# Performance work log

Measured on AMD Instinct MI355X. Metric: run time of the kernel, lower is better.

The kernel has to match this reference:

```python
import jax, jax.numpy as jnp
import numpy as np

N = 8192
D = 128
AVG_DEG = 32


def setup_inputs() -> dict:
    key = jax.random.key(0)
    ks = jax.random.split(key, 10)
    Z = jax.random.normal(ks[0], (N, D), dtype=jnp.float32)
    # random symmetric binary adjacency with avg degree ~ AVG_DEG
    p = AVG_DEG / N
    adj = (jax.random.uniform(ks[1], (N, N)) < p).astype(jnp.float32)
    adj = jnp.maximum(adj, adj.T)
    # symmetric normalized adjacency: D^{-1/2} A D^{-1/2}
    deg = adj.sum(axis=1)
    d_inv_sqrt = jnp.where(deg > 0, 1.0 / jnp.sqrt(deg), 0.0)
    A_norm = d_inv_sqrt[:, None] * adj * d_inv_sqrt[None, :]
    sc = 1.0 / np.sqrt(D)
    W_D = jax.random.uniform(ks[2], (D, D), minval=-sc, maxval=sc, dtype=jnp.float32)
    W_C = jax.random.uniform(ks[3], (D, D), minval=-sc, maxval=sc, dtype=jnp.float32)
    w_V = jax.random.uniform(ks[4], (D,), minval=-sc, maxval=sc, dtype=jnp.float32)
    W1 = jax.random.uniform(ks[5], (D, D), minval=-sc, maxval=sc, dtype=jnp.float32)
    b1 = jax.random.uniform(ks[6], (D,), minval=-sc, maxval=sc, dtype=jnp.float32)
    W2 = jax.random.uniform(ks[7], (D, D), minval=-sc, maxval=sc, dtype=jnp.float32)
    b2 = jax.random.uniform(ks[8], (D,), minval=-sc, maxval=sc, dtype=jnp.float32)
    omega_logit = jnp.float32(0.0)  # sigmoid -> 0.5
    delta_logit = jnp.float32(0.0)
    return {"Z": Z, "A_norm": A_norm, "W_D": W_D, "W_C": W_C, "w_V": w_V,
            "W1": W1, "b1": b1, "W2": W2, "b2": b2,
            "omega_logit": omega_logit, "delta_logit": delta_logit}


def reference(Z, A_norm, W_D, W_C, w_V, W1, b1, W2, b2, omega_logit, delta_logit):
    omega = jax.nn.sigmoid(omega_logit)
    delta = jax.nn.sigmoid(delta_logit)
    # Diffusion: ReLU(A_norm @ Z @ W_D^T)
    dif = jax.nn.relu(A_norm @ (Z @ W_D.T))  # [N, D]
    # Convection (standard attention). Since W_V is D->1,
    # W_V(z_i - z_j) == s_i - s_j with s = Z @ w_V -> avoid [N,N,D] tensor.
    s = Z @ w_V                                   # [N]
    V_bar = jax.nn.sigmoid(s[:, None] - s[None, :])  # [N, N]
    A = jax.nn.softmax(V_bar, axis=1)                # row-stochastic [N, N]
    con = A @ (Z @ W_C.T)                            # [N, D]
    # Reaction: nonlinear MLP
    rea = jnp.tanh(Z @ W1.T + b1) @ W2.T + b2        # [N, D]
    return omega * dif + (1.0 - omega) * con + delta * rea
```

## Files before the change

### kernel.cpp

```cpp
#include <hip/hip_runtime.h>
#include <hip/hip_bf16.h>
#include <stdint.h>

#define NN 8192
#define DD 128
#define MAXDEG 128

typedef float f32x4 __attribute__((ext_vector_type(4)));
typedef unsigned int u32x4 __attribute__((ext_vector_type(4)));
typedef __bf16 bf16x8 __attribute__((ext_vector_type(8)));
typedef __bf16 bf16x4 __attribute__((ext_vector_type(4)));

__device__ __forceinline__ f32x4 mfma16(bf16x8 a, bf16x8 b, f32x4 c) {
    return __builtin_amdgcn_mfma_f32_16x16x32_bf16(a, b, c, 0, 0, 0);
}

__device__ __forceinline__ bf16x8 pack8(f32x4 lo, f32x4 hi) {
    bf16x8 r;
    r[0] = (__bf16)lo[0]; r[1] = (__bf16)lo[1]; r[2] = (__bf16)lo[2]; r[3] = (__bf16)lo[3];
    r[4] = (__bf16)hi[0]; r[5] = (__bf16)hi[1]; r[6] = (__bf16)hi[2]; r[7] = (__bf16)hi[3];
    return r;
}

__device__ __forceinline__ float fast_sigmoid(float x) {
    return __builtin_amdgcn_rcpf(1.0f + __expf(-x));
}

__device__ __forceinline__ uint32_t f32_bf16bits_rne(float f) {
    union { float f; uint32_t u; } c; c.f = f;
    return (c.u + 0x7fffu + ((c.u >> 16) & 1u)) >> 16;
}

__device__ __forceinline__ float bf16bits_f32(uint32_t b) {
    union { uint32_t u; float f; } c; c.u = b << 16;
    return c.f;
}

__global__ __launch_bounds__(256) void k_prep_sE(
    const float* __restrict__ Z, const float* __restrict__ wV, float* __restrict__ E)
{
    const int wid  = threadIdx.x >> 6;
    const int lane = threadIdx.x & 63;
    const int row  = blockIdx.x * 4 + wid;
    float p = Z[row * DD + lane] * wV[lane] + Z[row * DD + 64 + lane] * wV[64 + lane];
    #pragma unroll
    for (int off = 32; off > 0; off >>= 1) p += __shfl_xor(p, off, 64);
    if (lane == 0) E[row] = __expf(p);
}

__global__ __launch_bounds__(256) void k_conv_w(
    const float* __restrict__ W_D, const float* __restrict__ W_C,
    const float* __restrict__ W1, const float* __restrict__ W2,
    __bf16* __restrict__ Wb)
{
    const int t = blockIdx.x * 256 + threadIdx.x;
    const int m = t >> 12, i = t & 4095;
    const float* src = (m == 0) ? W_D : (m == 1) ? W_C : (m == 2) ? W1 : W2;
    const f32x4 v = *(const f32x4*)(src + i * 4);
    bf16x4 b;
    b[0] = (__bf16)v[0]; b[1] = (__bf16)v[1]; b[2] = (__bf16)v[2]; b[3] = (__bf16)v[3];
    *(bf16x4*)(Wb + m * 16384 + i * 4) = b;
}

__global__ __launch_bounds__(256) void k_prep2(
    const float* __restrict__ Z, const __bf16* __restrict__ Wb,
    const float* __restrict__ b1, const float* __restrict__ b2,
    const float* __restrict__ delta_logit,
    __bf16* __restrict__ XR, __bf16* __restrict__ YB, __bf16* __restrict__ REA)
{
    __shared__ __bf16 Hs[32][136];
    const int tid = threadIdx.x;
    const int w = tid >> 6, l = tid & 63;
    const int lr = l & 15, lg = l >> 4;
    const int wr = w & 1, wn = w >> 1;
    const int r0 = blockIdx.x * 32;
    const int arow = r0 + 16 * wr + lr;
    const __bf16* WDb = Wb;
    const __bf16* WCb = Wb + 16384;
    const __bf16* W1b = Wb + 32768;
    const __bf16* W2b = Wb + 49152;

    const f32x4 zero4 = {0.f, 0.f, 0.f, 0.f};
    f32x4 aXD[4], aY[4], aH[4];
    #pragma unroll
    for (int i = 0; i < 4; ++i) { aXD[i] = zero4; aY[i] = zero4; aH[i] = zero4; }

    #pragma unroll
    for (int t = 0; t < 4; ++t) {
        const int k0 = 32 * t + 8 * lg;
        const bf16x8 af = pack8(*(const f32x4*)(Z + arow * DD + k0),
                                *(const f32x4*)(Z + arow * DD + k0 + 4));
        #pragma unroll
        for (int nf = 0; nf < 4; ++nf) {
            const int col = 64 * wn + 16 * nf + lr;
            aXD[nf] = mfma16(af, *(const bf16x8*)(WDb + col * DD + k0), aXD[nf]);
            aY[nf]  = mfma16(af, *(const bf16x8*)(WCb + col * DD + k0), aY[nf]);
            aH[nf]  = mfma16(af, *(const bf16x8*)(W1b + col * DD + k0), aH[nf]);
        }
    }

    const int orow = r0 + 16 * wr + 4 * lg;
    const int tile = orow >> 5;
    #pragma unroll
    for (int nf = 0; nf < 4; ++nf) {
        const int col = 64 * wn + 16 * nf + lr;
        bf16x4 yo;
        const float bb1 = b1[col];
        #pragma unroll
        for (int r = 0; r < 4; ++r) {
            XR[(orow + r) * DD + col] = (__bf16)aXD[nf][r];
            yo[r] = (__bf16)aY[nf][r];
            const float x = aH[nf][r] + bb1;
            const float e = __expf(2.0f * x);
            Hs[16 * wr + 4 * lg + r][col] = (__bf16)(1.0f - 2.0f * __builtin_amdgcn_rcpf(e + 1.0f));
        }
        *(bf16x4*)(YB + tile * 4096 + col * 32 + (orow & 31)) = yo;
    }
    __syncthreads();

    f32x4 aR[4];
    #pragma unroll
    for (int i = 0; i < 4; ++i) aR[i] = zero4;
    #pragma unroll
    for (int t = 0; t < 4; ++t) {
        const int k0 = 32 * t + 8 * lg;
        const bf16x8 hf = *(const bf16x8*)(&Hs[16 * wr + lr][k0]);
        #pragma unroll
        for (int nf = 0; nf < 4; ++nf) {
            const int col = 64 * wn + 16 * nf + lr;
            aR[nf] = mfma16(hf, *(const bf16x8*)(W2b + col * DD + k0), aR[nf]);
        }
    }
    const float delta = fast_sigmoid(delta_logit[0]);
    #pragma unroll
    for (int nf = 0; nf < 4; ++nf) {
        const int col = 64 * wn + 16 * nf + lr;
        const float bb2 = b2[col];
        #pragma unroll
        for (int r = 0; r < 4; ++r)
            REA[(orow + r) * DD + col] = (__bf16)(delta * (aR[nf][r] + bb2));
    }
}

__global__ __launch_bounds__(256) void k_scan(
    const float* __restrict__ A, uint32_t* __restrict__ cnt, uint32_t* __restrict__ ents)
{
    const int wid = threadIdx.x >> 6, lane = threadIdx.x & 63;
    const int row = blockIdx.x * 4 + wid;
    const float* rp = A + (size_t)row * NN + lane * 4;
    uint32_t* eb = ents + row * MAXDEG;
    uint32_t base = 0;
    #pragma unroll 4
    for (int i = 0; i < 32; ++i) {
        const f32x4 v = *(const f32x4*)(rp + i * 256);
        const int colb = i * 256 + lane * 4;
        #pragma unroll
        for (int k = 0; k < 4; ++k) {
            const bool nz = (v[k] != 0.0f);
            const unsigned long long m = __ballot(nz);
            if (nz) {
                const uint32_t pfx = __builtin_amdgcn_mbcnt_hi(
                    (uint32_t)(m >> 32), __builtin_amdgcn_mbcnt_lo((uint32_t)m, 0u));
                const uint32_t slot = base + pfx;
                if (slot < MAXDEG)
                    eb[slot] = ((uint32_t)(colb + k) << 16) | f32_bf16bits_rne(v[k]);
            }
            base += (uint32_t)__popcll(m);
        }
    }
    if (lane == 0) cnt[row] = base;
}

__global__ __launch_bounds__(512) __attribute__((amdgpu_waves_per_eu(2, 2))) void k_con(
    const float* __restrict__ E, const __bf16* __restrict__ YB,
    const __bf16* __restrict__ XR, const __bf16* __restrict__ REA,
    const uint32_t* __restrict__ cnt, const uint32_t* __restrict__ ents,
    const float* __restrict__ omega_logit, float* __restrict__ out)
{
    __shared__ float red[4][64][76];
    float* conS = &red[0][0][0];
    const int tid = threadIdx.x;
    const int w = tid >> 6, l = tid & 63;
    const int lr = l & 15, lg = l >> 4;
    const int r0 = blockIdx.x * 32;
    const int kstart = w * 1024;

    const float* ep = E + kstart + 8 * lg;
    const __bf16* yp = YB + (kstart >> 5) * 4096 + lr * 32 + 8 * lg;
    const float u0 = E[r0 + lr];
    const float u1 = E[r0 + 16 + lr];

    const f32x4 zero4 = {0.f, 0.f, 0.f, 0.f};
    f32x4 aC0[8], aC1[8], aden0 = zero4, aden1 = zero4;
    #pragma unroll
    for (int i = 0; i < 8; ++i) { aC0[i] = zero4; aC1[i] = zero4; }
    bf16x8 ones;
    #pragma unroll
    for (int i = 0; i < 8; ++i) ones[i] = (__bf16)1.0f;

    f32x4 eAa, eBa, eAb, eBb;
    bf16x8 bya[8], byb[8];
    intptr_t adv = 32;

#define LOADT(S) do {                                                         \
        eA##S = *(const f32x4*)(ep); eB##S = *(const f32x4*)(ep + 4);         \
        _Pragma("unroll")                                                     \
        for (int c = 0; c < 8; ++c) by##S[c] = *(const bf16x8*)(yp + c * 512);\
        ep += adv; yp += adv * 128;                                           \
    } while (0)

#define COMPT(S) do {                                                         \
        bf16x8 gf0, gf1;                                                      \
        _Pragma("unroll")                                                     \
        for (int j = 0; j < 4; ++j) {                                         \
            const float ea = eA##S[j], eb = eB##S[j];                         \
            gf0[j]     = (__bf16)__expf(u0 * __builtin_amdgcn_rcpf(u0 + ea)); \
            gf0[4 + j] = (__bf16)__expf(u0 * __builtin_amdgcn_rcpf(u0 + eb)); \
            gf1[j]     = (__bf16)__expf(u1 * __builtin_amdgcn_rcpf(u1 + ea)); \
            gf1[4 + j] = (__bf16)__expf(u1 * __builtin_amdgcn_rcpf(u1 + eb)); \
        }                                                                     \
        _Pragma("unroll")                                                     \
        for (int c = 0; c < 8; ++c) {                                         \
            aC0[c] = mfma16(gf0, by##S[c], aC0[c]);                           \
            aC1[c] = mfma16(gf1, by##S[c], aC1[c]);                           \
        }                                                                     \
        aden0 = mfma16(gf0, ones, aden0);                                     \
        aden1 = mfma16(gf1, ones, aden1);                                     \
    } while (0)

    LOADT(a);
    for (int it = 0; it < 16; ++it) {
        if (it == 15) adv = 0;
        LOADT(b); COMPT(a);
        LOADT(a); COMPT(b);
    }
#undef LOADT
#undef COMPT

#define STORE_ACC(dst) do {                                                   \
        _Pragma("unroll")                                                     \
        for (int c = 0; c < 8; ++c) {                                         \
            *(f32x4*)((dst) + c * 4)      = aC0[c];                           \
            *(f32x4*)((dst) + 36 + c * 4) = aC1[c];                           \
        }                                                                     \
        *(f32x4*)((dst) + 32)      = aden0;                                   \
        *(f32x4*)((dst) + 36 + 32) = aden1;                                   \
    } while (0)
#define ADD_ACC(src) do {                                                     \
        _Pragma("unroll")                                                     \
        for (int c = 0; c < 8; ++c) {                                         \
            aC0[c] += *(const f32x4*)((src) + c * 4);                         \
            aC1[c] += *(const f32x4*)((src) + 36 + c * 4);                    \
        }                                                                     \
        aden0 += *(const f32x4*)((src) + 32);                                 \
        aden1 += *(const f32x4*)((src) + 36 + 32);                            \
    } while (0)

    if (w >= 4) STORE_ACC(&red[w - 4][l][0]);
    __syncthreads();
    if (w < 4) ADD_ACC(&red[w][l][0]);
    __syncthreads();
    if (w == 2 || w == 3) STORE_ACC(&red[w - 2][l][0]);
    __syncthreads();
    if (w < 2) ADD_ACC(&red[w][l][0]);
    __syncthreads();
    if (w == 1) STORE_ACC(&red[0][l][0]);
    __syncthreads();
    if (w == 0) {
        ADD_ACC(&red[0][l][0]);
        __builtin_amdgcn_s_barrier();
        #pragma unroll
        for (int rf = 0; rf < 2; ++rf) {
            #pragma unroll
            for (int c = 0; c < 8; ++c) {
                const f32x4 v = rf ? aC1[c] : aC0[c];
                #pragma unroll
                for (int r = 0; r < 4; ++r)
                    conS[(16 * rf + 4 * lg + r) * 132 + 16 * c + lr] = v[r];
            }
            if (lr == 0) {
                const f32x4 d = rf ? aden1 : aden0;
                #pragma unroll
                for (int r = 0; r < 4; ++r)
                    conS[32 * 132 + 16 * rf + 4 * lg + r] = d[r];
            }
        }
    } else {
        __builtin_amdgcn_s_barrier();
    }
    __syncthreads();

    const int row = tid >> 4;
    const int g16 = tid & 15;
    const int col0 = 8 * g16;
    const int rg = r0 + row;
    float acc[8];
    #pragma unroll
    for (int i = 0; i < 8; ++i) acc[i] = 0.0f;

    const uint32_t n = min(cnt[rg], (uint32_t)MAXDEG);
    const uint32_t* ep2 = ents + rg * MAXDEG;
    uint32_t e = 0;
    for (; e + 4 <= n; e += 4) {
        const u32x4 p = *(const u32x4*)(ep2 + e);
        const bf16x8 x0 = *(const bf16x8*)(XR + (size_t)(p[0] >> 16) * DD + col0);
        const bf16x8 x1 = *(const bf16x8*)(XR + (size_t)(p[1] >> 16) * DD + col0);
        const bf16x8 x2 = *(const bf16x8*)(XR + (size_t)(p[2] >> 16) * DD + col0);
        const bf16x8 x3 = *(const bf16x8*)(XR + (size_t)(p[3] >> 16) * DD + col0);
        const float v0 = bf16bits_f32(p[0] & 0xffffu);
        const float v1 = bf16bits_f32(p[1] & 0xffffu);
        const float v2 = bf16bits_f32(p[2] & 0xffffu);
        const float v3 = bf16bits_f32(p[3] & 0xffffu);
        #pragma unroll
        for (int i = 0; i < 8; ++i)
            acc[i] += v0 * (float)x0[i] + v1 * (float)x1[i]
                    + v2 * (float)x2[i] + v3 * (float)x3[i];
    }
    for (; e < n; ++e) {
        const uint32_t p = ep2[e];
        const float val = bf16bits_f32(p & 0xffffu);
        const bf16x8 xv = *(const bf16x8*)(XR + (size_t)(p >> 16) * DD + col0);
        #pragma unroll
        for (int i = 0; i < 8; ++i) acc[i] += val * (float)xv[i];
    }

    const float omega = fast_sigmoid(omega_logit[0]);
    const float om1 = 1.0f - omega;
    const float dinv = __builtin_amdgcn_rcpf(conS[32 * 132 + row]);
    const bf16x8 rea8 = *(const bf16x8*)(REA + (size_t)rg * DD + col0);
    f32x4 o0, o1;
    #pragma unroll
    for (int i = 0; i < 8; ++i) {
        const float dv = fmaxf(acc[i], 0.0f);
        const float cv = conS[row * 132 + col0 + i] * dinv;
        const float v = (float)rea8[i] + omega * dv + om1 * cv;
        if (i < 4) o0[i] = v; else o1[i - 4] = v;
    }
    *(f32x4*)(out + (size_t)rg * DD + col0) = o0;
    *(f32x4*)(out + (size_t)rg * DD + col0 + 4) = o1;
}

extern "C" void kernel_launch(void* const* d_in, const int* in_sizes, int n_in,
                              void* d_out, int out_size, void* d_ws, size_t ws_size,
                              hipStream_t stream) {
    (void)in_sizes; (void)n_in; (void)out_size; (void)ws_size;
    const float* Z   = (const float*)d_in[0];
    const float* A   = (const float*)d_in[1];
    const float* W_D = (const float*)d_in[2];
    const float* W_C = (const float*)d_in[3];
    const float* wV  = (const float*)d_in[4];
    const float* W1  = (const float*)d_in[5];
    const float* b1  = (const float*)d_in[6];
    const float* W2  = (const float*)d_in[7];
    const float* b2  = (const float*)d_in[8];
    const float* omega_logit = (const float*)d_in[9];
    const float* delta_logit = (const float*)d_in[10];
    float* out = (float*)d_out;

    char* wsb = (char*)d_ws;
    float*    E    = (float*)wsb;
    __bf16*   Wb   = (__bf16*)(wsb + 32768);
    __bf16*   XR   = (__bf16*)(wsb + 163840);
    __bf16*   YB   = (__bf16*)(wsb + 163840 + 2097152);
    __bf16*   REA  = (__bf16*)(wsb + 163840 + 2 * 2097152);
    uint32_t* cnt  = (uint32_t*)(wsb + 163840 + 3 * 2097152);
    uint32_t* ents = (uint32_t*)(wsb + 163840 + 3 * 2097152 + 32768);

    k_prep_sE<<<dim3(2048), dim3(256), 0, stream>>>(Z, wV, E);
    k_conv_w<<<dim3(64), dim3(256), 0, stream>>>(W_D, W_C, W1, W2, Wb);
    k_prep2<<<dim3(256), dim3(256), 0, stream>>>(Z, Wb, b1, b2, delta_logit, XR, YB, REA);
    k_scan<<<dim3(2048), dim3(256), 0, stream>>>(A, cnt, ents);
    k_con<<<dim3(256), dim3(512), 0, stream>>>(E, YB, XR, REA, cnt, ents, omega_logit, out);
}
```

Baseline: 453.7 us.

## Fuse adjacency scan into main kernel with LDS neighbor lists; merge weight conversion

The adjacency-row scan now runs inside the main convection kernel: each block compacts its own 32 rows of A into shared-memory neighbor lists. This removes the separate scan launch and the global write and re-read of the count and entry arrays. Weight bf16 conversion is folded into the E-precompute kernel, dropping another launch. The trade-off is that the 256 MB scan now runs on far fewer waves (256 blocks, each wave handling four rows in turn), which may reduce memory-level parallelism. It also adds 16 KB of LDS per block.

```diff
diff --git a/kernel.cpp b/kernel.cpp
--- a/kernel.cpp
+++ b/kernel.cpp
@@ -36,8 +36,11 @@
     return c.f;
 }
 
-__global__ __launch_bounds__(256) void k_prep_sE(
-    const float* __restrict__ Z, const float* __restrict__ wV, float* __restrict__ E)
+__global__ __launch_bounds__(256) void k_prepA(
+    const float* __restrict__ Z, const float* __restrict__ wV,
+    const float* __restrict__ W_D, const float* __restrict__ W_C,
+    const float* __restrict__ W1, const float* __restrict__ W2,
+    float* __restrict__ E, __bf16* __restrict__ Wb)
 {
     const int wid  = threadIdx.x >> 6;
     const int lane = threadIdx.x & 63;
@@ -46,20 +49,16 @@
     #pragma unroll
     for (int off = 32; off > 0; off >>= 1) p += __shfl_xor(p, off, 64);
     if (lane == 0) E[row] = __expf(p);
-}
-
-__global__ __launch_bounds__(256) void k_conv_w(
-    const float* __restrict__ W_D, const float* __restrict__ W_C,
-    const float* __restrict__ W1, const float* __restrict__ W2,
-    __bf16* __restrict__ Wb)
-{
+
     const int t = blockIdx.x * 256 + threadIdx.x;
-    const int m = t >> 12, i = t & 4095;
-    const float* src = (m == 0) ? W_D : (m == 1) ? W_C : (m == 2) ? W1 : W2;
-    const f32x4 v = *(const f32x4*)(src + i * 4);
-    bf16x4 b;
-    b[0] = (__bf16)v[0]; b[1] = (__bf16)v[1]; b[2] = (__bf16)v[2]; b[3] = (__bf16)v[3];
-    *(bf16x4*)(Wb + m * 16384 + i * 4) = b;
+    if (t < 16384) {
+        const int m = t >> 12, i = t & 4095;
+        const float* src = (m == 0) ? W_D : (m == 1) ? W_C : (m == 2) ? W1 : W2;
+        const f32x4 v = *(const f32x4*)(src + i * 4);
+        bf16x4 b;
+        b[0] = (__bf16)v[0]; b[1] = (__bf16)v[1]; b[2] = (__bf16)v[2]; b[3] = (__bf16)v[3];
+        *(bf16x4*)(Wb + m * 16384 + i * 4) = b;
+    }
 }
 
 __global__ __launch_bounds__(256) void k_prep2(
@@ -142,49 +141,49 @@
     }
 }
 
-__global__ __launch_bounds__(256) void k_scan(
-    const float* __restrict__ A, uint32_t* __restrict__ cnt, uint32_t* __restrict__ ents)
-{
-    const int wid = threadIdx.x >> 6, lane = threadIdx.x & 63;
-    const int row = blockIdx.x * 4 + wid;
-    const float* rp = A + (size_t)row * NN + lane * 4;
-    uint32_t* eb = ents + row * MAXDEG;
-    uint32_t base = 0;
-    #pragma unroll 4
-    for (int i = 0; i < 32; ++i) {
-        const f32x4 v = *(const f32x4*)(rp + i * 256);
-        const int colb = i * 256 + lane * 4;
-        #pragma unroll
-        for (int k = 0; k < 4; ++k) {
-            const bool nz = (v[k] != 0.0f);
-            const unsigned long long m = __ballot(nz);
-            if (nz) {
-                const uint32_t pfx = __builtin_amdgcn_mbcnt_hi(
-                    (uint32_t)(m >> 32), __builtin_amdgcn_mbcnt_lo((uint32_t)m, 0u));
-                const uint32_t slot = base + pfx;
-                if (slot < MAXDEG)
-                    eb[slot] = ((uint32_t)(colb + k) << 16) | f32_bf16bits_rne(v[k]);
-            }
-            base += (uint32_t)__popcll(m);
-        }
-    }
-    if (lane == 0) cnt[row] = base;
-}
-
-__global__ __launch_bounds__(512) __attribute__((amdgpu_waves_per_eu(2, 2))) void k_con(
-    const float* __restrict__ E, const __bf16* __restrict__ YB,
-    const __bf16* __restrict__ XR, const __bf16* __restrict__ REA,
-    const uint32_t* __restrict__ cnt, const uint32_t* __restrict__ ents,
-    const float* __restrict__ omega_logit, float* __restrict__ out)
+__global__ __launch_bounds__(512) __attribute__((amdgpu_waves_per_eu(2, 2))) void k_main(
+    const float* __restrict__ A, const float* __restrict__ E,
+    const __bf16* __restrict__ YB, const __bf16* __restrict__ XR,
+    const __bf16* __restrict__ REA, const float* __restrict__ omega_logit,
+    float* __restrict__ out)
 {
     __shared__ float red[4][64][76];
+    __shared__ uint32_t ents_lds[32][MAXDEG];
+    __shared__ uint32_t cnt_lds[32];
     float* conS = &red[0][0][0];
     const int tid = threadIdx.x;
     const int w = tid >> 6, l = tid & 63;
     const int lr = l & 15, lg = l >> 4;
     const int r0 = blockIdx.x * 32;
+
+    for (int j = 0; j < 4; ++j) {
+        const int rrow = 4 * w + j;
+        const float* rp = A + (size_t)(r0 + rrow) * NN + l * 4;
+        uint32_t* eb = &ents_lds[rrow][0];
+        uint32_t base = 0;
+        #pragma unroll 4
+        for (int i = 0; i < 32; ++i) {
+            const f32x4 v = *(const f32x4*)(rp + i * 256);
+            const int colb = i * 256 + l * 4;
+            #pragma unroll
+            for (int k = 0; k < 4; ++k) {
+                const bool nz = (v[k] != 0.0f);
+                const unsigned long long m = __ballot(nz);
+                if (nz) {
+                    const uint32_t pfx = __builtin_amdgcn_mbcnt_hi(
+                        (uint32_t)(m >> 32), __builtin_amdgcn_mbcnt_lo((uint32_t)m, 0u));
+                    const uint32_t slot = base + pfx;
+                    if (slot < MAXDEG)
+                        eb[slot] = ((uint32_t)(colb + k) << 16) | f32_bf16bits_rne(v[k]);
+                }
+                base += (uint32_t)__popcll(m);
+            }
+        }
+        if (l == 0) cnt_lds[rrow] = min(base, (uint32_t)MAXDEG);
+    }
+    __syncthreads();
+
     const int kstart = w * 1024;
-
     const float* ep = E + kstart + 8 * lg;
     const __bf16* yp = YB + (kstart >> 5) * 4096 + lr * 32 + 8 * lg;
     const float u0 = E[r0 + lr];
@@ -298,8 +297,8 @@
     #pragma unroll
     for (int i = 0; i < 8; ++i) acc[i] = 0.0f;
 
-    const uint32_t n = min(cnt[rg], (uint32_t)MAXDEG);
-    const uint32_t* ep2 = ents + rg * MAXDEG;
+    const uint32_t n = cnt_lds[row];
+    const uint32_t* ep2 = &ents_lds[row][0];
     uint32_t e = 0;
     for (; e + 4 <= n; e += 4) {
         const u32x4 p = *(const u32x4*)(ep2 + e);
@@ -358,17 +357,13 @@
     float* out = (float*)d_out;
 
     char* wsb = (char*)d_ws;
-    float*    E    = (float*)wsb;
-    __bf16*   Wb   = (__bf16*)(wsb + 32768);
-    __bf16*   XR   = (__bf16*)(wsb + 163840);
-    __bf16*   YB   = (__bf16*)(wsb + 163840 + 2097152);
-    __bf16*   REA  = (__bf16*)(wsb + 163840 + 2 * 2097152);
-    uint32_t* cnt  = (uint32_t*)(wsb + 163840 + 3 * 2097152);
-    uint32_t* ents = (uint32_t*)(wsb + 163840 + 3 * 2097152 + 32768);
-
-    k_prep_sE<<<dim3(2048), dim3(256), 0, stream>>>(Z, wV, E);
-    k_conv_w<<<dim3(64), dim3(256), 0, stream>>>(W_D, W_C, W1, W2, Wb);
+    float*  E   = (float*)wsb;
+    __bf16* Wb  = (__bf16*)(wsb + 32768);
+    __bf16* XR  = (__bf16*)(wsb + 163840);
+    __bf16* YB  = (__bf16*)(wsb + 163840 + 2097152);
+    __bf16* REA = (__bf16*)(wsb + 163840 + 2 * 2097152);
+
+    k_prepA<<<dim3(2048), dim3(256), 0, stream>>>(Z, wV, W_D, W_C, W1, W2, E, Wb);
     k_prep2<<<dim3(256), dim3(256), 0, stream>>>(Z, Wb, b1, b2, delta_logit, XR, YB, REA);
-    k_scan<<<dim3(2048), dim3(256), 0, stream>>>(A, cnt, ents);
-    k_con<<<dim3(256), dim3(512), 0, stream>>>(E, YB, XR, REA, cnt, ents, omega_logit, out);
-}
+    k_main<<<dim3(256), dim3(512), 0, stream>>>(A, E, YB, XR, REA, omega_logit, out);
+}
```

Result: no change. 460.4 us (+1.5%).
